# Optimization experiments

Measured on AMD Instinct MI355X. Metric: run time of the kernel, lower is better.

## Reference

```python
import jax, jax.numpy as jnp
import numpy as np

B, D, T, H, E = 4, 1024, 2048, 16, 64  # batch, dim, seq_len, n_heads, hidden_dim (H*E == D)


def setup_inputs() -> dict:
    key = jax.random.key(0)
    ks = jax.random.split(key, 6)
    x = jax.random.normal(ks[0], (B, D, T), dtype=jnp.float32)            # (b, e, t) layout
    Wp = jax.random.normal(ks[1], (H, E, D), dtype=jnp.float32) / np.sqrt(D)  # per-head proj weights
    bp = jax.random.normal(ks[2], (H, E), dtype=jnp.float32) * 0.01
    tw = jax.random.normal(ks[3], (H, T), dtype=jnp.float32) / np.sqrt(T)  # per-head Toeplitz kernel, tw[h,0]=diagonal
    Wo = jax.random.normal(ks[4], (D, D), dtype=jnp.float32) / np.sqrt(D)
    bo = jax.random.normal(ks[5], (D,), dtype=jnp.float32) * 0.01
    return {"x": x, "Wp": Wp, "bp": bp, "tw": tw, "Wo": Wo, "bo": bo}


def reference(x, Wp, bp, tw, Wo, bo):
    # x: (b, dim, t) -> (b, t, dim)
    xt = jnp.transpose(x, (0, 2, 1))
    # per-head projections: (b, h, e, t)
    proj = jnp.einsum('btd,hed->bhet', xt, Wp) + bp[None, :, :, None]
    # build per-head causal lower-triangular Toeplitz matrices: Tm[h, t, s] = tw[h, t-s] if s <= t else 0
    idx = jnp.arange(T)[:, None] - jnp.arange(T)[None, :]  # (t, s)
    Tm = jnp.where(idx >= 0, tw[:, jnp.clip(idx, 0)], 0.0)  # (h, t, s)
    # causal Toeplitz mixing along time per head
    mixed = jnp.einsum('hts,bhes->bhet', Tm, proj)          # (b, h, e, t)
    # concat heads on feature dim: (b, t, h*e) == (b, t, dim)
    cat = jnp.transpose(mixed, (0, 3, 1, 2)).reshape(B, T, H * E)
    out = cat @ Wo.T + bo                                   # out_proj: Linear(dim, dim)
    return jnp.transpose(out, (0, 2, 1))                    # back to (b, e, t)
```

## Files before the change

kernel.cpp:

```cpp
#include <hip/hip_runtime.h>
#include <cstdint>

#define NB 4
#define ND 1024
#define NT 2048
#define NH 16
#define NE 64
#define GLEN 2240
#define CAP 2312

typedef __bf16 bf16x8 __attribute__((ext_vector_type(8)));
typedef float f32x4 __attribute__((ext_vector_type(4)));
typedef unsigned short us8 __attribute__((ext_vector_type(8)));

__device__ __forceinline__ unsigned short f2bf(float f) {
  unsigned u = __builtin_bit_cast(unsigned, f);
  return (unsigned short)((u + 0x7fffu + ((u >> 16) & 1u)) >> 16);
}

__device__ __forceinline__ void gload16(const void* g, void* l) {
  __builtin_amdgcn_global_load_lds(
      (const __attribute__((address_space(1))) void*)(uintptr_t)g,
      (__attribute__((address_space(3))) void*)(uintptr_t)l, 16, 0, 0);
}

__global__ void prep_kernel(const float* __restrict__ Wp, const float* __restrict__ Wo,
                            const float* __restrict__ tw,
                            unsigned short* __restrict__ WpB, unsigned short* __restrict__ WoB,
                            unsigned short* __restrict__ Gr8) {
  int idx = blockIdx.x * 256 + threadIdx.x;
  int stride = gridDim.x * 256;
  for (int i = idx; i < ND * ND; i += stride) WpB[i] = f2bf(Wp[i]);
  for (int i = idx; i < ND * ND; i += stride) WoB[i] = f2bf(Wo[i]);
  for (int i = idx; i < NH * 8 * GLEN; i += stride) {
    int h = i / (8 * GLEN);
    int rem = i - h * 8 * GLEN;
    int r = rem / GLEN;
    int c = rem - r * GLEN;
    int src = c + r;
    Gr8[i] = (src <= NT - 1) ? f2bf(tw[h * NT + (NT - 1) - src]) : (unsigned short)0;
  }
}

__global__ __launch_bounds__(256) void transpose_cast(const float* __restrict__ x,
                                                      unsigned short* __restrict__ xT) {
  __shared__ float tile[32][33];
  int tx = threadIdx.x & 31, ty = threadIdx.x >> 5;
  int t0 = blockIdx.x * 32, d0 = blockIdx.y * 32, b = blockIdx.z;
  const float* xb = x + (long)b * ND * NT;
#pragma unroll
  for (int k = 0; k < 4; ++k)
    tile[ty + 8 * k][tx] = xb[(long)(d0 + ty + 8 * k) * NT + t0 + tx];
  __syncthreads();
  unsigned short* xTb = xT + (long)b * NT * ND;
#pragma unroll
  for (int k = 0; k < 4; ++k)
    xTb[(long)(t0 + ty + 8 * k) * ND + d0 + tx] = f2bf(tile[tx][ty + 8 * k]);
}

template <bool OUT_BF16>
__global__ __launch_bounds__(256, 2) void gemm_bt(const unsigned short* __restrict__ A,
                                                  const unsigned short* __restrict__ Bt,
                                                  const float* __restrict__ bias,
                                                  void* __restrict__ Cb, long strideB,
                                                  long strideC) {
  const int N = 2048, K = 1024;
  __shared__ __align__(16) unsigned short As[128 * 32];
  __shared__ __align__(16) unsigned short Bs[128 * 32];
  const int tid = threadIdx.x;
  const int lane = tid & 63;
  const int wid = tid >> 6;
  const int wm = (wid & 1) * 64, wn = (wid >> 1) * 64;
  const int m0 = blockIdx.y * 128, n0 = blockIdx.x * 128;
  const unsigned short* Bb = Bt + (long)blockIdx.z * strideB;
  const int mlo = lane & 15, q = lane >> 4;

  f32x4 acc[4][4] = {};
  for (int k0 = 0; k0 < K; k0 += 32) {
#pragma unroll
    for (int p = 0; p < 2; ++p) {
      int idx = p * 256 + tid;
      int row = idx >> 2, kc = (idx & 3) * 8;
      gload16(A + (long)(m0 + row) * K + k0 + kc, &As[idx * 8]);
      gload16(Bb + (long)(n0 + row) * K + k0 + kc, &Bs[idx * 8]);
    }
    __syncthreads();
    bf16x8 av[4], bv[4];
#pragma unroll
    for (int i = 0; i < 4; ++i) {
      av[i] = __builtin_bit_cast(bf16x8, *(const us8*)&As[(wm + i * 16 + mlo) * 32 + q * 8]);
      bv[i] = __builtin_bit_cast(bf16x8, *(const us8*)&Bs[(wn + i * 16 + mlo) * 32 + q * 8]);
    }
#pragma unroll
    for (int i = 0; i < 4; ++i)
#pragma unroll
      for (int j = 0; j < 4; ++j)
        acc[i][j] = __builtin_amdgcn_mfma_f32_16x16x32_bf16(av[i], bv[j], acc[i][j], 0, 0, 0);
    __syncthreads();
  }
#pragma unroll
  for (int i = 0; i < 4; ++i)
#pragma unroll
    for (int j = 0; j < 4; ++j)
#pragma unroll
      for (int r = 0; r < 4; ++r) {
        int gr = m0 + wm + i * 16 + q * 4 + r;
        int gc = n0 + wn + j * 16 + mlo;
        float v = acc[i][j][r] + bias[gr];
        if (OUT_BF16)
          ((unsigned short*)Cb)[(long)blockIdx.z * strideC + (long)gr * N + gc] = f2bf(v);
        else
          ((float*)Cb)[(long)blockIdx.z * strideC + (long)gr * N + gc] = v;
      }
}

__global__ __launch_bounds__(256, 2) void toeplitz(const unsigned short* __restrict__ proj,
                                                   const unsigned short* __restrict__ Gr8,
                                                   unsigned short* __restrict__ mixedT) {
  __shared__ __align__(16) unsigned short Ls[8 * CAP];
  __shared__ __align__(16) unsigned short Bs[2][64 * 32];
  const int tid = threadIdx.x, lane = tid & 63, w = tid >> 6;
  const int j = blockIdx.x, h = blockIdx.y, bz = blockIdx.z;
  const int mlo = lane & 15, q = lane >> 4;
  const int wt = (w >> 1) * 64, we = (w & 1) * 32;
  const int t0L = (15 - j) * 128, t0S = j * 128;

  const int delta = (NT - 128) - t0L;
  const int MUSE = t0L + 256;
#pragma unroll 1
  for (int r = 0; r < 8; ++r) {
    int rr = (r + delta) & 7;
    int off8 = r + delta - rr;
    const unsigned short* src = Gr8 + (long)(h * 8 + rr) * GLEN + off8;
    unsigned short* dst = &Ls[r * CAP];
    for (int mc = tid; mc * 8 < MUSE; mc += 256) gload16(src + mc * 8, dst + mc * 8);
  }

  const int rA = (7 - mlo) & 7;
  const int eRow = tid >> 2, kCol = (tid & 3) * 8;
  const unsigned short* bsrc = proj + ((long)bz * ND + h * 64 + eRow) * NT + kCol;

#pragma unroll 1
  for (int p = 0; p < 2; ++p) {
    const int t0p = p ? t0S : t0L;
    const int kend = t0p + 128;
    const unsigned short* lA =
        &Ls[rA * CAP + (127 - wt - mlo - rA) + q * 8 + (t0L - t0p)];
    gload16(bsrc, &Bs[0][tid * 8]);
    __syncthreads();
    bf16x8 ap0 = __builtin_bit_cast(bf16x8, *(const us8*)(lA - 32));
    bf16x8 ap1 = __builtin_bit_cast(bf16x8, *(const us8*)(lA - 48));
    f32x4 acc[4][2] = {};
#pragma unroll 1
    for (int s0 = 0; s0 < kend; s0 += 64) {
      gload16(bsrc + s0 + 32, &Bs[1][tid * 8]);
      {
        bf16x8 a0 = __builtin_bit_cast(bf16x8, *(const us8*)(lA + s0));
        bf16x8 a1 = __builtin_bit_cast(bf16x8, *(const us8*)(lA + s0 - 16));
        bf16x8 b0 = __builtin_bit_cast(bf16x8, *(const us8*)&Bs[0][(we + mlo) * 32 + q * 8]);
        bf16x8 b1 = __builtin_bit_cast(bf16x8, *(const us8*)&Bs[0][(we + 16 + mlo) * 32 + q * 8]);
        acc[0][0] = __builtin_amdgcn_mfma_f32_16x16x32_bf16(a0, b0, acc[0][0], 0, 0, 0);
        acc[0][1] = __builtin_amdgcn_mfma_f32_16x16x32_bf16(a0, b1, acc[0][1], 0, 0, 0);
        acc[1][0] = __builtin_amdgcn_mfma_f32_16x16x32_bf16(a1, b0, acc[1][0], 0, 0, 0);
        acc[1][1] = __builtin_amdgcn_mfma_f32_16x16x32_bf16(a1, b1, acc[1][1], 0, 0, 0);
        acc[2][0] = __builtin_amdgcn_mfma_f32_16x16x32_bf16(ap0, b0, acc[2][0], 0, 0, 0);
        acc[2][1] = __builtin_amdgcn_mfma_f32_16x16x32_bf16(ap0, b1, acc[2][1], 0, 0, 0);
        acc[3][0] = __builtin_amdgcn_mfma_f32_16x16x32_bf16(ap1, b0, acc[3][0], 0, 0, 0);
        acc[3][1] = __builtin_amdgcn_mfma_f32_16x16x32_bf16(ap1, b1, acc[3][1], 0, 0, 0);
        ap0 = a0;
        ap1 = a1;
      }
      __syncthreads();
      if (s0 + 64 < kend) gload16(bsrc + s0 + 64, &Bs[0][tid * 8]);
      {
        bf16x8 a0 = __builtin_bit_cast(bf16x8, *(const us8*)(lA + s0 + 32));
        bf16x8 a1 = __builtin_bit_cast(bf16x8, *(const us8*)(lA + s0 + 16));
        bf16x8 b0 = __builtin_bit_cast(bf16x8, *(const us8*)&Bs[1][(we + mlo) * 32 + q * 8]);
        bf16x8 b1 = __builtin_bit_cast(bf16x8, *(const us8*)&Bs[1][(we + 16 + mlo) * 32 + q * 8]);
        acc[0][0] = __builtin_amdgcn_mfma_f32_16x16x32_bf16(a0, b0, acc[0][0], 0, 0, 0);
        acc[0][1] = __builtin_amdgcn_mfma_f32_16x16x32_bf16(a0, b1, acc[0][1], 0, 0, 0);
        acc[1][0] = __builtin_amdgcn_mfma_f32_16x16x32_bf16(a1, b0, acc[1][0], 0, 0, 0);
        acc[1][1] = __builtin_amdgcn_mfma_f32_16x16x32_bf16(a1, b1, acc[1][1], 0, 0, 0);
        acc[2][0] = __builtin_amdgcn_mfma_f32_16x16x32_bf16(ap0, b0, acc[2][0], 0, 0, 0);
        acc[2][1] = __builtin_amdgcn_mfma_f32_16x16x32_bf16(ap0, b1, acc[2][1], 0, 0, 0);
        acc[3][0] = __builtin_amdgcn_mfma_f32_16x16x32_bf16(ap1, b0, acc[3][0], 0, 0, 0);
        acc[3][1] = __builtin_amdgcn_mfma_f32_16x16x32_bf16(ap1, b1, acc[3][1], 0, 0, 0);
        ap0 = a0;
        ap1 = a1;
      }
      __syncthreads();
    }
#pragma unroll
    for (int i = 0; i < 4; ++i)
#pragma unroll
      for (int jj = 0; jj < 2; ++jj)
#pragma unroll
        for (int rr = 0; rr < 4; ++rr) {
          int t = t0p + wt + i * 16 + q * 4 + rr;
          int e = we + jj * 16 + mlo;
          mixedT[((long)bz * NT + t) * ND + h * 64 + e] = f2bf(acc[i][jj][rr]);
        }
  }
}

extern "C" void kernel_launch(void* const* d_in, const int* in_sizes, int n_in, void* d_out,
                              int out_size, void* d_ws, size_t ws_size, hipStream_t stream) {
  const float* x = (const float*)d_in[0];
  const float* Wp = (const float*)d_in[1];
  const float* bp = (const float*)d_in[2];
  const float* tw = (const float*)d_in[3];
  const float* Wo = (const float*)d_in[4];
  const float* bo = (const float*)d_in[5];
  float* out = (float*)d_out;

  char* ws = (char*)d_ws;
  unsigned short* xT = (unsigned short*)(ws);
  unsigned short* proj = (unsigned short*)(ws + (16ull << 20));
  unsigned short* WpB = (unsigned short*)(ws + (32ull << 20));
  unsigned short* WoB = (unsigned short*)(ws + (34ull << 20));
  unsigned short* Gr8 = (unsigned short*)(ws + (36ull << 20));

  prep_kernel<<<dim3(2048), 256, 0, stream>>>(Wp, Wo, tw, WpB, WoB, Gr8);
  transpose_cast<<<dim3(NT / 32, ND / 32, NB), 256, 0, stream>>>(x, xT);
  gemm_bt<true><<<dim3(16, 8, NB), 256, 0, stream>>>(WpB, xT, bp, proj, (long)NT * ND,
                                                     (long)ND * NT);
  toeplitz<<<dim3(8, NH, NB), 256, 0, stream>>>(proj, Gr8, xT);
  gemm_bt<false><<<dim3(16, 8, NB), 256, 0, stream>>>(WoB, xT, bo, out, (long)NT * ND,
                                                      (long)ND * NT);
}
```

Baseline: 176.4 us.

## Double-buffer GEMM LDS tiles and vectorize cast and transpose kernels

```diff
diff --git a/kernel.cpp b/kernel.cpp
--- a/kernel.cpp
+++ b/kernel.cpp
@@ -12,6 +12,7 @@
 typedef __bf16 bf16x8 __attribute__((ext_vector_type(8)));
 typedef float f32x4 __attribute__((ext_vector_type(4)));
 typedef unsigned short us8 __attribute__((ext_vector_type(8)));
+typedef unsigned short us4 __attribute__((ext_vector_type(4)));
 
 __device__ __forceinline__ unsigned short f2bf(float f) {
   unsigned u = __builtin_bit_cast(unsigned, f);
@@ -30,8 +31,17 @@
                             unsigned short* __restrict__ Gr8) {
   int idx = blockIdx.x * 256 + threadIdx.x;
   int stride = gridDim.x * 256;
-  for (int i = idx; i < ND * ND; i += stride) WpB[i] = f2bf(Wp[i]);
-  for (int i = idx; i < ND * ND; i += stride) WoB[i] = f2bf(Wo[i]);
+  const int n4 = ND * ND / 4;
+  for (int i = idx; i < n4; i += stride) {
+    float4 v = ((const float4*)Wp)[i];
+    us4 o = {f2bf(v.x), f2bf(v.y), f2bf(v.z), f2bf(v.w)};
+    ((us4*)WpB)[i] = o;
+  }
+  for (int i = idx; i < n4; i += stride) {
+    float4 v = ((const float4*)Wo)[i];
+    us4 o = {f2bf(v.x), f2bf(v.y), f2bf(v.z), f2bf(v.w)};
+    ((us4*)WoB)[i] = o;
+  }
   for (int i = idx; i < NH * 8 * GLEN; i += stride) {
     int h = i / (8 * GLEN);
     int rem = i - h * 8 * GLEN;
@@ -44,29 +54,38 @@
 
 __global__ __launch_bounds__(256) void transpose_cast(const float* __restrict__ x,
                                                       unsigned short* __restrict__ xT) {
-  __shared__ float tile[32][33];
-  int tx = threadIdx.x & 31, ty = threadIdx.x >> 5;
-  int t0 = blockIdx.x * 32, d0 = blockIdx.y * 32, b = blockIdx.z;
+  __shared__ float tile[64][65];
+  const int c = threadIdx.x & 15, r = threadIdx.x >> 4;
+  const int t0 = blockIdx.x * 64, d0 = blockIdx.y * 64, b = blockIdx.z;
   const float* xb = x + (long)b * ND * NT;
 #pragma unroll
-  for (int k = 0; k < 4; ++k)
-    tile[ty + 8 * k][tx] = xb[(long)(d0 + ty + 8 * k) * NT + t0 + tx];
+  for (int k = 0; k < 4; ++k) {
+    float4 v = *(const float4*)&xb[(long)(d0 + r + 16 * k) * NT + t0 + 4 * c];
+    tile[r + 16 * k][4 * c + 0] = v.x;
+    tile[r + 16 * k][4 * c + 1] = v.y;
+    tile[r + 16 * k][4 * c + 2] = v.z;
+    tile[r + 16 * k][4 * c + 3] = v.w;
+  }
   __syncthreads();
   unsigned short* xTb = xT + (long)b * NT * ND;
 #pragma unroll
-  for (int k = 0; k < 4; ++k)
-    xTb[(long)(t0 + ty + 8 * k) * ND + d0 + tx] = f2bf(tile[tx][ty + 8 * k]);
+  for (int k = 0; k < 4; ++k) {
+    int t = r + 16 * k;
+    us4 o = {f2bf(tile[4 * c + 0][t]), f2bf(tile[4 * c + 1][t]), f2bf(tile[4 * c + 2][t]),
+             f2bf(tile[4 * c + 3][t])};
+    *(us4*)&xTb[(long)(t0 + t) * ND + d0 + 4 * c] = o;
+  }
 }
 
 template <bool OUT_BF16>
-__global__ __launch_bounds__(256, 2) void gemm_bt(const unsigned short* __restrict__ A,
+__global__ __launch_bounds__(256, 3) void gemm_bt(const unsigned short* __restrict__ A,
                                                   const unsigned short* __restrict__ Bt,
                                                   const float* __restrict__ bias,
                                                   void* __restrict__ Cb, long strideB,
                                                   long strideC) {
   const int N = 2048, K = 1024;
-  __shared__ __align__(16) unsigned short As[128 * 32];
-  __shared__ __align__(16) unsigned short Bs[128 * 32];
+  __shared__ __align__(16) unsigned short As[2][128 * 32];
+  __shared__ __align__(16) unsigned short Bs[2][128 * 32];
   const int tid = threadIdx.x;
   const int lane = tid & 63;
   const int wid = tid >> 6;
@@ -76,27 +95,38 @@
   const int mlo = lane & 15, q = lane >> 4;
 
   f32x4 acc[4][4] = {};
-  for (int k0 = 0; k0 < K; k0 += 32) {
+  auto stage = [&](int buf, int k0) {
 #pragma unroll
     for (int p = 0; p < 2; ++p) {
       int idx = p * 256 + tid;
       int row = idx >> 2, kc = (idx & 3) * 8;
-      gload16(A + (long)(m0 + row) * K + k0 + kc, &As[idx * 8]);
-      gload16(Bb + (long)(n0 + row) * K + k0 + kc, &Bs[idx * 8]);
+      gload16(A + (long)(m0 + row) * K + k0 + kc, &As[buf][idx * 8]);
+      gload16(Bb + (long)(n0 + row) * K + k0 + kc, &Bs[buf][idx * 8]);
     }
-    __syncthreads();
+  };
+  auto compute = [&](int buf) {
     bf16x8 av[4], bv[4];
 #pragma unroll
     for (int i = 0; i < 4; ++i) {
-      av[i] = __builtin_bit_cast(bf16x8, *(const us8*)&As[(wm + i * 16 + mlo) * 32 + q * 8]);
-      bv[i] = __builtin_bit_cast(bf16x8, *(const us8*)&Bs[(wn + i * 16 + mlo) * 32 + q * 8]);
+      av[i] = __builtin_bit_cast(bf16x8, *(const us8*)&As[buf][(wm + i * 16 + mlo) * 32 + q * 8]);
+      bv[i] = __builtin_bit_cast(bf16x8, *(const us8*)&Bs[buf][(wn + i * 16 + mlo) * 32 + q * 8]);
     }
 #pragma unroll
     for (int i = 0; i < 4; ++i)
 #pragma unroll
       for (int j = 0; j < 4; ++j)
         acc[i][j] = __builtin_amdgcn_mfma_f32_16x16x32_bf16(av[i], bv[j], acc[i][j], 0, 0, 0);
+  };
+
+  stage(0, 0);
+#pragma unroll 1
+  for (int k0 = 0; k0 < K; k0 += 64) {
     __syncthreads();
+    stage(1, k0 + 32);
+    compute(0);
+    __syncthreads();
+    if (k0 + 64 < K) stage(0, k0 + 64);
+    compute(1);
   }
 #pragma unroll
   for (int i = 0; i < 4; ++i)
@@ -144,8 +174,7 @@
   for (int p = 0; p < 2; ++p) {
     const int t0p = p ? t0S : t0L;
     const int kend = t0p + 128;
-    const unsigned short* lA =
-        &Ls[rA * CAP + (127 - wt - mlo - rA) + q * 8 + (t0L - t0p)];
+    const unsigned short* lA = &Ls[rA * CAP + (127 - wt - mlo - rA) + q * 8 + (t0L - t0p)];
     gload16(bsrc, &Bs[0][tid * 8]);
     __syncthreads();
     bf16x8 ap0 = __builtin_bit_cast(bf16x8, *(const us8*)(lA - 32));
@@ -220,8 +249,8 @@
   unsigned short* WoB = (unsigned short*)(ws + (34ull << 20));
   unsigned short* Gr8 = (unsigned short*)(ws + (36ull << 20));
 
-  prep_kernel<<<dim3(2048), 256, 0, stream>>>(Wp, Wo, tw, WpB, WoB, Gr8);
-  transpose_cast<<<dim3(NT / 32, ND / 32, NB), 256, 0, stream>>>(x, xT);
+  prep_kernel<<<dim3(1024), 256, 0, stream>>>(Wp, Wo, tw, WpB, WoB, Gr8);
+  transpose_cast<<<dim3(NT / 64, ND / 64, NB), 256, 0, stream>>>(x, xT);
   gemm_bt<true><<<dim3(16, 8, NB), 256, 0, stream>>>(WpB, xT, bp, proj, (long)NT * ND,
                                                      (long)ND * NT);
   toeplitz<<<dim3(8, NH, NB), 256, 0, stream>>>(proj, Gr8, xT);
```

Result: faster. 169.4 us (-4.0%).
